# Kernel tuning notes

Measured on AMD Instinct MI355X. Metric: run time of the kernel, lower is better.

Reference implementation:

```python
import jax, jax.numpy as jnp
import numpy as np

B, T, V, E, L, H = 128, 512, 128, 64, 128, 512  # batch, seq, vocab, char_emb, latent, hidden


def setup_inputs() -> dict:
    key = jax.random.key(0)
    ks = jax.random.split(key, 12)
    r = lambda k, shape, s=0.05: jax.random.normal(k, shape, dtype=jnp.float32) * s
    return {
        "char_ids": jax.random.randint(ks[0], (B, T), 0, V),
        "z": jax.random.normal(ks[1], (B, L), dtype=jnp.float32),
        "emb": r(ks[2], (V, E)),
        "cw1": r(ks[3], (L, H)), "cb1": jnp.zeros((H,)), "cg1": jnp.ones((H,)), "cbeta1": jnp.zeros((H,)),
        "cw2": r(ks[4], (H, H)), "cb2": jnp.zeros((H,)), "cg2": jnp.ones((H,)), "cbeta2": jnp.zeros((H,)),
        "wih0": r(ks[5], (4 * H, E + H + 2)), "whh0": r(ks[6], (4 * H, H)),
        "bih0": jnp.zeros((4 * H,)), "bhh0": jnp.zeros((4 * H,)),
        "wih1": r(ks[7], (4 * H, H)), "whh1": r(ks[8], (4 * H, H)),
        "bih1": jnp.zeros((4 * H,)), "bhh1": jnp.zeros((4 * H,)),
        "wo1": r(ks[9], (H, H // 2)), "bo1": jnp.zeros((H // 2,)),
        "wo2": r(ks[10], (H // 2, 2)), "bo2": jnp.zeros((2,)),
        "init_timing": jnp.zeros((2,)),
    }


def _ln(x, g, b, eps=1e-5):
    m = jnp.mean(x, -1, keepdims=True)
    v = jnp.var(x, -1, keepdims=True)
    return (x - m) * jax.lax.rsqrt(v + eps) * g + b


def _lstm_cell(x, h, c, wih, whh, bih, bhh):
    # PyTorch gate order: i, f, g, o
    gates = x @ wih.T + bih + h @ whh.T + bhh
    i, f, g, o = jnp.split(gates, 4, axis=-1)
    c = jax.nn.sigmoid(f) * c + jax.nn.sigmoid(i) * jnp.tanh(g)
    h = jax.nn.sigmoid(o) * jnp.tanh(c)
    return h, c


def reference(char_ids, z, emb, cw1, cb1, cg1, cbeta1, cw2, cb2, cg2, cbeta2,
              wih0, whh0, bih0, bhh0, wih1, whh1, bih1, bhh1,
              wo1, bo1, wo2, bo2, init_timing):
    b = char_ids.shape[0]
    # condition encoder: Linear -> LN -> LeakyReLU(0.2), twice
    cond = jax.nn.leaky_relu(_ln(z @ cw1 + cb1, cg1, cbeta1), 0.2)
    cond = jax.nn.leaky_relu(_ln(cond @ cw2 + cb2, cg2, cbeta2), 0.2)  # (B, H)
    xs = jnp.transpose(emb[char_ids], (1, 0, 2))  # (T, B, E)
    h0 = jnp.zeros((b, H), jnp.float32)
    c0 = jnp.zeros((b, H), jnp.float32)
    h1 = jnp.zeros((b, H), jnp.float32)
    c1 = jnp.zeros((b, H), jnp.float32)
    prev = jnp.broadcast_to(init_timing, (b, 2))

    def step(carry, xt):
        h0, c0, h1, c1, prev = carry
        xin = jnp.concatenate([xt, cond, prev], axis=-1)  # (B, E+H+2)
        h0, c0 = _lstm_cell(xin, h0, c0, wih0, whh0, bih0, bhh0)
        h1, c1 = _lstm_cell(h0, h1, c1, wih1, whh1, bih1, bhh1)
        out = jax.nn.leaky_relu(h1 @ wo1 + bo1, 0.2) @ wo2 + bo2
        out = jax.nn.softplus(out) + 0.005  # (B, 2)
        return (h0, c0, h1, c1, out), out

    _, ys = jax.lax.scan(step, (h0, c0, h1, c1, prev), xs)
    return jnp.transpose(ys, (1, 0, 2))  # (B, T, 2)
```

## Files before the change

### kernel.cpp

```cpp
#include <hip/hip_runtime.h>

#define Bn 128
#define Tn 512
#define Vn 128
#define En 64
#define Ln 128
#define Hn 512
#define G4 2048
#define WGS 256
#define NTHR 512
#define NALL (WGS * NTHR)
#define LSTR 520
#define GRPS 8
#define WPG 32
#define RPG 16

typedef unsigned short u16;
typedef unsigned int u32;
typedef __bf16 bf16x8 __attribute__((ext_vector_type(8)));
typedef float f32x4 __attribute__((ext_vector_type(4)));
typedef u32 u32x4 __attribute__((ext_vector_type(4)));

__device__ inline float bf2f(u16 h) {
    u32 u = ((u32)h) << 16;
    float f;
    __builtin_memcpy(&f, &u, 4);
    return f;
}
__device__ inline u16 f2bf(float f) {
    u32 u;
    __builtin_memcpy(&u, &f, 4);
    u32 r = (u + 0x7fffu + ((u >> 16) & 1u)) >> 16;
    return (u16)r;
}
__device__ inline u32 f2u(float f) { u32 u; __builtin_memcpy(&u, &f, 4); return u; }
__device__ inline float u2f(u32 u) { float f; __builtin_memcpy(&f, &u, 4); return f; }
__device__ inline float sigm(float x) { return 1.f / (1.f + expf(-x)); }
__device__ inline float leaky(float x) { return x > 0.f ? x : 0.2f * x; }
__device__ inline float softplus(float x) {
    return x > 0.f ? x + log1pf(expf(-x)) : log1pf(expf(x));
}

__device__ inline void cload16(const u32* p, u32* w) {
    u32x4 v0, v1, v2, v3;
    asm volatile(
        "global_load_dwordx4 %0, %4, off sc0 sc1\n\t"
        "global_load_dwordx4 %1, %4, off offset:16 sc0 sc1\n\t"
        "global_load_dwordx4 %2, %4, off offset:32 sc0 sc1\n\t"
        "global_load_dwordx4 %3, %4, off offset:48 sc0 sc1\n\t"
        "s_waitcnt vmcnt(0)"
        : "=&v"(v0), "=&v"(v1), "=&v"(v2), "=&v"(v3)
        : "v"(p)
        : "memory");
    *(u32x4*)(w) = v0;
    *(u32x4*)(w + 4) = v1;
    *(u32x4*)(w + 8) = v2;
    *(u32x4*)(w + 12) = v3;
}
__device__ inline u32 cload1(const u32* p) {
    u32 v;
    asm volatile("global_load_dword %0, %1, off sc0 sc1\n\ts_waitcnt vmcnt(0)"
                 : "=v"(v) : "v"(p) : "memory");
    return v;
}
__device__ inline void cwait() { asm volatile("s_waitcnt vmcnt(0)" ::: "memory"); }
__device__ inline void cstore1(u32* p, u32 v) {
    asm volatile("global_store_dword %0, %1, off sc0 sc1" :: "v"(p), "v"(v) : "memory");
}

#define OFF_FLAGS  0x000000
#define OFF_B1SUM  0x002000
#define OFF_WP     0x004000
#define OFF_BIAS0  0x008000
#define OFF_CPAR   0x00A000
#define OFF_H0P    0x010000
#define OFF_H1P    0x050000
#define OFF_PART   0x090000
#define OFF_WO1TH  0x0B0000
#define OFF_WO1TL  0x0F0000
#define OFF_ZF     0x130000
#define OFF_CW1F   0x140000
#define OFF_CW2F   0x180000
#define OFF_CONDF  0x280000
#define OFF_YBUF   0x2C0000
#define OFF_BASE0  0x300000
#define OFF_EMBW   0x400000
#define OFF_W0HI   0x500000
#define OFF_W0LO   0x700000
#define OFF_W1HI   0x900000
#define OFF_W1LO   0xB00000
#define OFF_WI1HI  0xD00000
#define OFF_WI1LO  0xF00000

__device__ inline void gbar_heavy(int* cnt, int* gen) {
    __syncthreads();
    if (threadIdx.x == 0) {
        __threadfence();
        int g = __hip_atomic_load(gen, __ATOMIC_RELAXED, __HIP_MEMORY_SCOPE_AGENT);
        int arrived = __hip_atomic_fetch_add(cnt, 1, __ATOMIC_ACQ_REL, __HIP_MEMORY_SCOPE_AGENT);
        if (arrived == WGS - 1) {
            __hip_atomic_store(cnt, 0, __ATOMIC_RELAXED, __HIP_MEMORY_SCOPE_AGENT);
            __hip_atomic_store(gen, g + 1, __ATOMIC_RELEASE, __HIP_MEMORY_SCOPE_AGENT);
        } else {
            while (__hip_atomic_load(gen, __ATOMIC_ACQUIRE, __HIP_MEMORY_SCOPE_AGENT) == g)
                __builtin_amdgcn_s_sleep(1);
        }
        __threadfence();
    }
    __syncthreads();
}

__device__ inline void poll32(const u32* gf, u32 sq) {
    const int l = threadIdx.x & 31;
    for (;;) {
        u32 v = cload1(gf + l);
        if (__all((int)(v >= sq))) break;
        __builtin_amdgcn_s_sleep(4);
    }
}
__device__ inline void poll16(const u32* gf, u32 sq) {
    const int l = threadIdx.x & 15;
    for (;;) {
        u32 v = cload1(gf + l);
        if (__all((int)(v >= sq))) break;
        __builtin_amdgcn_s_sleep(4);
    }
}

__device__ inline void unpack16(const u32* w, u16* ph, u16* pl) {
    u32 hd[8], ld[8];
#pragma unroll
    for (int i = 0; i < 8; ++i) {
        hd[i] = (w[2 * i] & 0xFFFFu) | (w[2 * i + 1] << 16);
        ld[i] = (w[2 * i] >> 16) | (w[2 * i + 1] & 0xFFFF0000u);
    }
    *(u32x4*)(ph) = *(const u32x4*)(hd);
    *(u32x4*)(ph + 8) = *(const u32x4*)(hd + 4);
    *(u32x4*)(pl) = *(const u32x4*)(ld);
    *(u32x4*)(pl + 8) = *(const u32x4*)(ld + 4);
}

#define MF(a, b, c) __builtin_amdgcn_mfma_f32_16x16x32_bf16(a, b, c, 0, 0, 0)

__device__ inline f32x4 gemm16_3(const u16* __restrict__ Ah, const u16* __restrict__ Al,
                                 const u16* __restrict__ Bhb, const u16* __restrict__ Blb,
                                 int colb, int n, int q) {
    const u16* Bh = Bhb + (size_t)(colb + n) * Hn;
    const u16* Bl = Blb + (size_t)(colb + n) * Hn;
    const int a0 = n * LSTR;
    f32x4 c0 = {0.f, 0.f, 0.f, 0.f}, c1 = c0, c2 = c0;
#pragma unroll 4
    for (int it = 0; it < 16; ++it) {
        const int ko = it * 32 + q * 8;
        bf16x8 bh = *(const bf16x8*)(Bh + ko);
        bf16x8 bl = *(const bf16x8*)(Bl + ko);
        bf16x8 ah = *(const bf16x8*)(Ah + a0 + ko);
        bf16x8 al = *(const bf16x8*)(Al + a0 + ko);
        c0 = MF(ah, bh, c0);
        c1 = MF(al, bh, c1);
        c2 = MF(ah, bl, c2);
    }
    return c0 + c1 + c2;
}

__device__ inline f32x4 gemm16_regB(const u16* __restrict__ Ah, const u16* __restrict__ Al,
                                    const bf16x8* wbh, const bf16x8* wbl, int n, int q) {
    const int a0 = n * LSTR;
    f32x4 c0 = {0.f, 0.f, 0.f, 0.f}, c1 = c0, c2 = c0;
#pragma unroll
    for (int it = 0; it < 16; ++it) {
        const int ko = it * 32 + q * 8;
        bf16x8 ah = *(const bf16x8*)(Ah + a0 + ko);
        bf16x8 al = *(const bf16x8*)(Al + a0 + ko);
        c0 = MF(ah, wbh[it], c0);
        c1 = MF(al, wbh[it], c1);
        c2 = MF(ah, wbl[it], c2);
    }
    return c0 + c1 + c2;
}

__device__ inline f32x4 gemm16_ldsB(const u16* __restrict__ Ah, const u16* __restrict__ Al,
                                    const u16* __restrict__ Bh, const u16* __restrict__ Bl,
                                    int n, int q) {
    const int a0 = n * LSTR;
    f32x4 c0 = {0.f, 0.f, 0.f, 0.f}, c1 = c0, c2 = c0;
#pragma unroll 4
    for (int it = 0; it < 16; ++it) {
        const int ko = it * 32 + q * 8;
        bf16x8 bh = *(const bf16x8*)(Bh + a0 + ko);
        bf16x8 bl = *(const bf16x8*)(Bl + a0 + ko);
        bf16x8 ah = *(const bf16x8*)(Ah + a0 + ko);
        bf16x8 al = *(const bf16x8*)(Al + a0 + ko);
        c0 = MF(ah, bh, c0);
        c1 = MF(al, bh, c1);
        c2 = MF(ah, bl, c2);
    }
    return c0 + c1 + c2;
}

__device__ inline void stage(float* dst, const void* src, int n, int gtid, bool isbf) {
    if (isbf) {
        const u16* s = (const u16*)src;
        for (int e = gtid; e < n; e += NALL) dst[e] = bf2f(s[e]);
    } else {
        const float* s = (const float*)src;
        for (int e = gtid; e < n; e += NALL) dst[e] = s[e];
    }
}
__device__ inline void stage_split(u16* hi, u16* lo, const void* src, int n, int gtid, bool isbf) {
    if (isbf) {
        const u16* s = (const u16*)src;
        for (int e = gtid; e < n; e += NALL) { hi[e] = s[e]; lo[e] = 0; }
    } else {
        const float* s = (const float*)src;
        for (int e = gtid; e < n; e += NALL) {
            float w = s[e];
            u16 h = f2bf(w);
            hi[e] = h;
            lo[e] = f2bf(w - bf2f(h));
        }
    }
}

template <bool ISBF>
__device__ inline float ldw(const void* p, size_t i) {
    if constexpr (ISBF) return bf2f(((const u16*)p)[i]);
    else return ((const float*)p)[i];
}

template <bool ISBF>
__device__ void phase5(const void* wih0, const void* emb, const float* __restrict__ condf,
                       const float* __restrict__ bias0f, float* __restrict__ base0,
                       float* __restrict__ embW, int gtid) {
    const int cc = gtid & 2047;
    const int bb0 = gtid >> 11;
    float b = bias0f[cc];
    float a0 = b, a1 = b, a2 = b, a3 = b;
    const float* c0p = condf + (size_t)bb0 * Hn;
    const float* c1p = condf + (size_t)(bb0 + 32) * Hn;
    const float* c2p = condf + (size_t)(bb0 + 64) * Hn;
    const float* c3p = condf + (size_t)(bb0 + 96) * Hn;
    const size_t wb = (size_t)cc * 578 + 64;
    for (int k = 0; k < Hn; ++k) {
        float w = ldw<ISBF>(wih0, wb + k);
        a0 += c0p[k] * w; a1 += c1p[k] * w; a2 += c2p[k] * w; a3 += c3p[k] * w;
    }
    base0[(size_t)bb0 * G4 + cc] = a0;
    base0[(size_t)(bb0 + 32) * G4 + cc] = a1;
    base0[(size_t)(bb0 + 64) * G4 + cc] = a2;
    base0[(size_t)(bb0 + 96) * G4 + cc] = a3;
    float e0 = 0.f, e1 = 0.f, e2 = 0.f, e3 = 0.f;
    const size_t wb2 = (size_t)cc * 578;
    for (int k = 0; k < En; ++k) {
        float w = ldw<ISBF>(wih0, wb2 + k);
        e0 += ldw<ISBF>(emb, (size_t)bb0 * En + k) * w;
        e1 += ldw<ISBF>(emb, (size_t)(bb0 + 32) * En + k) * w;
        e2 += ldw<ISBF>(emb, (size_t)(bb0 + 64) * En + k) * w;
        e3 += ldw<ISBF>(emb, (size_t)(bb0 + 96) * En + k) * w;
    }
    embW[(size_t)bb0 * G4 + cc] = e0;
    embW[(size_t)(bb0 + 32) * G4 + cc] = e1;
    embW[(size_t)(bb0 + 64) * G4 + cc] = e2;
    embW[(size_t)(bb0 + 96) * G4 + cc] = e3;
}

__device__ inline void ln_leaky_row(const float* __restrict__ x, const float* __restrict__ gamma,
                                    const float* __restrict__ beta, float* __restrict__ out,
                                    float* red) {
    int tid = threadIdx.x;
    float v = x[tid];
    float s = v, s2 = v * v;
    for (int off = 32; off; off >>= 1) {
        s += __shfl_down(s, off);
        s2 += __shfl_down(s2, off);
    }
    int wv = tid >> 6;
    if ((tid & 63) == 0) { red[wv * 2] = s; red[wv * 2 + 1] = s2; }
    __syncthreads();
    if (tid == 0) {
        float ts = 0.f, ts2 = 0.f;
        for (int i = 0; i < 8; ++i) { ts += red[i * 2]; ts2 += red[i * 2 + 1]; }
        float m = ts / 512.f;
        float var = ts2 / 512.f - m * m;
        red[16] = m;
        red[17] = rsqrtf(var + 1e-5f);
    }
    __syncthreads();
    float m = red[16], rs = red[17];
    out[tid] = leaky((v - m) * rs * gamma[tid] + beta[tid]);
    __syncthreads();
}

__global__ void init_flags_kernel(int* flags) { flags[threadIdx.x] = 0; }

__global__ __launch_bounds__(NTHR, 2) void gen_kernel(
    const int* __restrict__ char_ids, const void* z, const void* emb,
    const void* cw1, const void* cb1, const void* cg1, const void* cbeta1,
    const void* cw2, const void* cb2, const void* cg2, const void* cbeta2,
    const void* wih0, const void* whh0, const void* bih0, const void* bhh0,
    const void* wih1, const void* whh1, const void* bih1, const void* bhh1,
    const void* wo1, const void* bo1, const void* wo2, const void* bo2,
    const void* init_t, void* outp, char* __restrict__ ws) {
    __shared__ u16 lh0h[RPG * LSTR];
    __shared__ u16 lh0l[RPG * LSTR];
    __shared__ u16 lh1h[RPG * LSTR];
    __shared__ u16 lh1l[RPG * LSTR];
    __shared__ u16 lwoh[16 * LSTR];
    __shared__ u16 lwol[16 * LSTR];
    __shared__ float smemx[1024];
    __shared__ float pvs[32];
    __shared__ float red[34];

    int* flags = (int*)(ws + OFF_FLAGS);
    float* b1sum = (float*)(ws + OFF_B1SUM);
    float* wpb = (float*)(ws + OFF_WP);
    float* bias0f = (float*)(ws + OFF_BIAS0);
    float* cpar = (float*)(ws + OFF_CPAR);
    u32* h0p = (u32*)(ws + OFF_H0P);
    u32* h1p = (u32*)(ws + OFF_H1P);
    float* partf = (float*)(ws + OFF_PART);
    u16* wo1Th = (u16*)(ws + OFF_WO1TH);
    u16* wo1Tl = (u16*)(ws + OFF_WO1TL);
    float* zf = (float*)(ws + OFF_ZF);
    float* cw1f = (float*)(ws + OFF_CW1F);
    float* cw2f = (float*)(ws + OFF_CW2F);
    float* condf = (float*)(ws + OFF_CONDF);
    float* ybuf = (float*)(ws + OFF_YBUF);
    float* base0 = (float*)(ws + OFF_BASE0);
    float* embW = (float*)(ws + OFF_EMBW);
    u16* W0hi = (u16*)(ws + OFF_W0HI);
    u16* W0lo = (u16*)(ws + OFF_W0LO);
    u16* W1hi = (u16*)(ws + OFF_W1HI);
    u16* W1lo = (u16*)(ws + OFF_W1LO);
    u16* Wi1hi = (u16*)(ws + OFF_WI1HI);
    u16* Wi1lo = (u16*)(ws + OFF_WI1LO);
    float* wo1f = base0;

    const bool isbf = (((const u32*)cg1)[0] == 0x3F803F80u);

    const int g = blockIdx.x;
    const int tid = threadIdx.x;
    const int wv = tid >> 6;
    const int grp = g >> 5;
    const int ut = g & 31;
    const int mat = wv >> 2;
    const int gw = wv & 3;
    const int R0g = grp * RPG;
    const int colb = gw * 512 + ut * 16;
    const int lane = tid & 63;
    const int n = lane & 15;
    const int q = lane >> 4;
    const int gtid = g * NTHR + tid;
    const f32x4 Z4 = {0.f, 0.f, 0.f, 0.f};

    u32* gf = (u32*)flags + grp * 64;
    u32* gf2 = (u32*)flags + grp * 64 + 32;
    u32* gfl = gf + ut;
    int* hcnt = flags + 512;
    int* hgen = flags + 528;
    float* part = partf + grp * 1024;

    stage_split(W0hi, W0lo, whh0, G4 * Hn, gtid, isbf);
    stage_split(W1hi, W1lo, whh1, G4 * Hn, gtid, isbf);
    stage_split(Wi1hi, Wi1lo, wih1, G4 * Hn, gtid, isbf);
    stage(zf, z, Bn * Ln, gtid, isbf);
    stage(cw1f, cw1, Ln * Hn, gtid, isbf);
    stage(cw2f, cw2, Hn * Hn, gtid, isbf);
    stage(cpar + 0, cg1, 512, gtid, isbf);
    stage(cpar + 512, cbeta1, 512, gtid, isbf);
    stage(cpar + 1024, cg2, 512, gtid, isbf);
    stage(cpar + 1536, cbeta2, 512, gtid, isbf);
    stage(cpar + 2048, bo1, 256, gtid, isbf);
    stage(cpar + 2304, bo2, 2, gtid, isbf);
    stage(cpar + 2560, cb2, 512, gtid, isbf);
    stage(cpar + 3072, cb1, 512, gtid, isbf);
    stage(cpar + 3584, wo2, 256 * 2, gtid, isbf);
    stage(wo1f, wo1, Hn * 256, gtid, isbf);
    if (gtid < Bn * Hn) { cstore1(h0p + gtid, 0); cstore1(h1p + gtid, 0); }
    if (isbf) {
        if (gtid < G4) b1sum[gtid] = bf2f(((const u16*)bih1)[gtid]) + bf2f(((const u16*)bhh1)[gtid]);
        if (gtid < G4) bias0f[gtid] = bf2f(((const u16*)bih0)[gtid]) + bf2f(((const u16*)bhh0)[gtid]);
        if (gtid < 4096) {
            size_t ix = (size_t)(gtid >> 1) * 578 + 576 + (gtid & 1);
            wpb[gtid] = bf2f(((const u16*)wih0)[ix]);
        }
    } else {
        if (gtid < G4) b1sum[gtid] = ((const float*)bih1)[gtid] + ((const float*)bhh1)[gtid];
        if (gtid < G4) bias0f[gtid] = ((const float*)bih0)[gtid] + ((const float*)bhh0)[gtid];
        if (gtid < 4096) {
            size_t ix = (size_t)(gtid >> 1) * 578 + 576 + (gtid & 1);
            wpb[gtid] = ((const float*)wih0)[ix];
        }
    }
    gbar_heavy(hcnt, hgen);
    if (gtid < Bn * Hn) {
        int bb = gtid >> 9, nn = gtid & 511;
        float a = cpar[3072 + nn];
        const float* zr = zf + bb * Ln;
        for (int k = 0; k < Ln; ++k) a += zr[k] * cw1f[k * Hn + nn];
        ybuf[gtid] = a;
    }
    for (int e = gtid; e < 256 * Hn; e += NALL) {
        int nn = e >> 9, kk = e & 511;
        float w = wo1f[kk * 256 + nn];
        u16 hv = f2bf(w);
        wo1Th[e] = hv;
        wo1Tl[e] = f2bf(w - bf2f(hv));
    }
    gbar_heavy(hcnt, hgen);
    if (g < Bn) ln_leaky_row(ybuf + g * Hn, cpar + 0, cpar + 512, condf + g * Hn, red);
    gbar_heavy(hcnt, hgen);
    if (g < Bn) {
        float a = cpar[2560 + tid];
        const float* crow = condf + g * Hn;
        for (int k = 0; k < Hn; ++k) a += crow[k] * cw2f[k * Hn + tid];
        ybuf[g * Hn + tid] = a;
    }
    gbar_heavy(hcnt, hgen);
    if (g < Bn) ln_leaky_row(ybuf + g * Hn, cpar + 1024, cpar + 1536, condf + g * Hn, red);
    gbar_heavy(hcnt, hgen);
    if (gtid < Bn * Hn) {
        if (isbf) phase5<true>(wih0, emb, condf, bias0f, base0, embW, gtid);
        else phase5<false>(wih0, emb, condf, bias0f, base0, embW, gtid);
    }
    gbar_heavy(hcnt, hgen);

    bf16x8 wbh[16], wbl[16];
    {
        const u16* Bh = (mat == 0 ? W0hi : W1hi) + (size_t)(colb + n) * Hn;
        const u16* Bl = (mat == 0 ? W0lo : W1lo) + (size_t)(colb + n) * Hn;
#pragma unroll
        for (int it = 0; it < 16; ++it) {
            wbh[it] = *(const bf16x8*)(Bh + it * 32 + q * 8);
            wbl[it] = *(const bf16x8*)(Bl + it * 32 + q * 8);
        }
    }
    const bool headwg = (ut < 16);
    if (headwg) {
        for (int e = tid; e < 16 * Hn; e += NTHR) {
            int col = e >> 9, k = e & 511;
            lwoh[col * LSTR + k] = wo1Th[(size_t)(ut * 16 + col) * Hn + k];
            lwol[col * LSTR + k] = wo1Tl[(size_t)(ut * 16 + col) * Hn + k];
        }
    }

    float c0 = 0.f, c1 = 0.f;
    const int lr = tid >> 4;
    const int un = tid & 15;
    const int bb = R0g + lr;
    const int uu = ut * 16 + un;
    const float* bo1f = cpar + 2048;
    const float* bo2f = cpar + 2304;
    const float* wo2f = cpar + 3584;
    const int srow = tid >> 5;
    const int blk = tid & 31;
    const int kub = blk * 16;
    f32x4 acc1c = Z4;

    for (int e = tid; e < RPG * LSTR; e += NTHR) {
        lh0h[e] = 0; lh0l[e] = 0; lh1h[e] = 0; lh1l[e] = 0;
    }
    if (tid < 32) pvs[tid] = isbf ? bf2f(((const u16*)init_t)[tid & 1])
                                  : ((const float*)init_t)[tid & 1];

    for (int t = 0; t < Tn; ++t) {
        if (t >= 1) {
            if (wv == 0) poll32(gf, 2 * (u32)t);
            __syncthreads();
            if (blk != ut) {
                u32 w[16];
                cload16(h1p + (size_t)(R0g + srow) * Hn + kub, w);
                unpack16(w, lh1h + srow * LSTR + kub, lh1l + srow * LSTR + kub);
            }
        }
        __syncthreads();
        if (headwg && wv == 0 && t >= 1) {
            f32x4 ha = gemm16_ldsB(lh1h, lh1l, lwoh, lwol, n, q);
            float p[4][2];
#pragma unroll
            for (int r = 0; r < 4; ++r) {
                float hv = leaky(ha[r] + bo1f[ut * 16 + n]);
                p[r][0] = hv * wo2f[(ut * 16 + n) * 2];
                p[r][1] = hv * wo2f[(ut * 16 + n) * 2 + 1];
            }
#pragma unroll
            for (int r = 0; r < 4; ++r)
#pragma unroll
                for (int j = 0; j < 2; ++j) {
                    float s = p[r][j];
                    s += __shfl_xor(s, 1, 16);
                    s += __shfl_xor(s, 2, 16);
                    s += __shfl_xor(s, 4, 16);
                    s += __shfl_xor(s, 8, 16);
                    p[r][j] = s;
                }
            if (n == 0) {
#pragma unroll
                for (int r = 0; r < 4; ++r)
#pragma unroll
                    for (int j = 0; j < 2; ++j) {
                        int row = q * 4 + r;
                        cstore1((u32*)(part + (row * 2 + j) * 16 + ut), f2u(p[r][j]));
                    }
            }
            cwait();
            if (tid == 0) cstore1(gf2 + ut, (u32)t);
        }
        if (mat == 0) {
            f32x4 a = gemm16_regB(lh0h, lh0l, wbh, wbl, n, q);
#pragma unroll
            for (int r = 0; r < 4; ++r)
                smemx[gw * 256 + (q * 4 + r) * 16 + n] = a[r];
        } else {
            acc1c = gemm16_regB(lh1h, lh1l, wbh, wbl, n, q);
        }
        if (t >= 1) {
            if (wv == 0) {
                poll16(gf2, (u32)t);
                if (tid < 32) {
                    int row = tid >> 1, j = tid & 1;
                    u32 hw[16];
                    cload16((const u32*)(part + (row * 2 + j) * 16), hw);
                    float s = bo2f[j];
#pragma unroll
                    for (int i = 0; i < 16; ++i) s += u2f(hw[i]);
                    float y = softplus(s) + 0.005f;
                    pvs[row * 2 + j] = y;
                    if (ut == 0) {
                        size_t oi = ((size_t)(R0g + row) * Tn + (t - 1)) * 2 + j;
                        if (isbf) ((u16*)outp)[oi] = f2bf(y);
                        else ((float*)outp)[oi] = y;
                    }
                }
            }
        }
        __syncthreads();
        if (tid < 256) {
            int id = char_ids[bb * Tn + t];
            float pv0 = pvs[lr * 2], pv1 = pvs[lr * 2 + 1];
            float gv[4];
#pragma unroll
            for (int gi = 0; gi < 4; ++gi) {
                int cc = gi * 512 + uu;
                gv[gi] = smemx[gi * 256 + lr * 16 + un] + base0[(size_t)bb * G4 + cc] +
                         embW[(size_t)id * G4 + cc] + pv0 * wpb[2 * cc] + pv1 * wpb[2 * cc + 1];
            }
            float ig = sigm(gv[0]), fg = sigm(gv[1]), gg = tanhf(gv[2]), og = sigm(gv[3]);
            c0 = fg * c0 + ig * gg;
            float h = og * tanhf(c0);
            u16 hv = f2bf(h);
            u16 lv = f2bf(h - bf2f(hv));
            lh0h[lr * LSTR + uu] = hv;
            lh0l[lr * LSTR + uu] = lv;
            cstore1(h0p + (size_t)bb * Hn + uu, (u32)hv | ((u32)lv << 16));
        }
        cwait();
        __syncthreads();
        if (tid == 0) cstore1(gfl, 2 * (u32)t + 1);

        if (wv == 0) poll32(gf, 2 * (u32)t + 1);
        __syncthreads();
        if (blk != ut) {
            u32 w[16];
            cload16(h0p + (size_t)(R0g + srow) * Hn + kub, w);
            unpack16(w, lh0h + srow * LSTR + kub, lh0l + srow * LSTR + kub);
        }
        __syncthreads();
        if (mat == 1) {
            f32x4 a = gemm16_3(lh0h, lh0l, Wi1hi, Wi1lo, colb, n, q);
            acc1c = acc1c + a;
#pragma unroll
            for (int r = 0; r < 4; ++r)
                smemx[gw * 256 + (q * 4 + r) * 16 + n] = acc1c[r];
        }
        __syncthreads();
        if (tid < 256) {
            float gv[4];
#pragma unroll
            for (int gi = 0; gi < 4; ++gi) {
                int cc = gi * 512 + uu;
                gv[gi] = smemx[gi * 256 + lr * 16 + un] + b1sum[cc];
            }
            float ig = sigm(gv[0]), fg = sigm(gv[1]), gg = tanhf(gv[2]), og = sigm(gv[3]);
            c1 = fg * c1 + ig * gg;
            float h = og * tanhf(c1);
            u16 hv = f2bf(h);
            u16 lv = f2bf(h - bf2f(hv));
            lh1h[lr * LSTR + uu] = hv;
            lh1l[lr * LSTR + uu] = lv;
            cstore1(h1p + (size_t)bb * Hn + uu, (u32)hv | ((u32)lv << 16));
        }
        cwait();
        __syncthreads();
        if (tid == 0) cstore1(gfl, 2 * (u32)t + 2);
    }

    if (wv == 0) poll32(gf, 2 * (u32)Tn);
    __syncthreads();
    if (blk != ut) {
        u32 w[16];
        cload16(h1p + (size_t)(R0g + srow) * Hn + kub, w);
        unpack16(w, lh1h + srow * LSTR + kub, lh1l + srow * LSTR + kub);
    }
    __syncthreads();
    if (headwg && wv == 0) {
        f32x4 ha = gemm16_ldsB(lh1h, lh1l, lwoh, lwol, n, q);
        float p[4][2];
#pragma unroll
        for (int r = 0; r < 4; ++r) {
            float hv = leaky(ha[r] + bo1f[ut * 16 + n]);
            p[r][0] = hv * wo2f[(ut * 16 + n) * 2];
            p[r][1] = hv * wo2f[(ut * 16 + n) * 2 + 1];
        }
#pragma unroll
        for (int r = 0; r < 4; ++r)
#pragma unroll
            for (int j = 0; j < 2; ++j) {
                float s = p[r][j];
                s += __shfl_xor(s, 1, 16);
                s += __shfl_xor(s, 2, 16);
                s += __shfl_xor(s, 4, 16);
                s += __shfl_xor(s, 8, 16);
                p[r][j] = s;
            }
        if (n == 0) {
#pragma unroll
            for (int r = 0; r < 4; ++r)
#pragma unroll
                for (int j = 0; j < 2; ++j) {
                    int row = q * 4 + r;
                    cstore1((u32*)(part + (row * 2 + j) * 16 + ut), f2u(p[r][j]));
                }
        }
        cwait();
        if (tid == 0) cstore1(gf2 + ut, (u32)Tn);
    }
    if (ut == 0 && wv == 0) {
        poll16(gf2, (u32)Tn);
        if (tid < 32) {
            int row = tid >> 1, j = tid & 1;
            u32 hw[16];
            cload16((const u32*)(part + (row * 2 + j) * 16), hw);
            float s = bo2f[j];
#pragma unroll
            for (int i = 0; i < 16; ++i) s += u2f(hw[i]);
            float y = softplus(s) + 0.005f;
            size_t oi = ((size_t)(R0g + row) * Tn + (Tn - 1)) * 2 + j;
            if (isbf) ((u16*)outp)[oi] = f2bf(y);
            else ((float*)outp)[oi] = y;
        }
    }
}

extern "C" void kernel_launch(void* const* d_in, const int* in_sizes, int n_in,
                              void* d_out, int out_size, void* d_ws, size_t ws_size,
                              hipStream_t stream) {
    (void)in_sizes; (void)n_in; (void)out_size; (void)ws_size;
    init_flags_kernel<<<1, 1024, 0, stream>>>((int*)d_ws);
    gen_kernel<<<WGS, NTHR, 0, stream>>>(
        (const int*)d_in[0], d_in[1], d_in[2], d_in[3], d_in[4], d_in[5], d_in[6], d_in[7],
        d_in[8], d_in[9], d_in[10], d_in[11], d_in[12], d_in[13], d_in[14], d_in[15], d_in[16],
        d_in[17], d_in[18], d_in[19], d_in[20], d_in[21], d_in[22], d_in[23],
        d_out, (char*)d_ws);
}
```

Baseline: 8.805 ms.

## Specialize bf16 path: keep all weights in registers, drop lo-weight MFMAs, remap groups

When inputs are bf16, the weight lo halves are zero, so the MFMA against the weight lo part is skipped. The freed register slot now holds Wi1 (for layer-1 waves) or the wo1 head weights, instead of streaming Wi1 from global memory and wo1 from LDS each step. It also remaps workgroups so the 8 row groups are interleaved across block indices, and moves the output-head reduction from wave 0 to wave 4 to balance work. The fp32 path keeps the old three-MFMA scheme.

Result: slower. 10.19 ms (+15.7%).

```diff
diff --git a/kernel.cpp b/kernel.cpp
--- a/kernel.cpp
+++ b/kernel.cpp
@@ -163,8 +163,8 @@
     return c0 + c1 + c2;
 }
 
-__device__ inline f32x4 gemm16_regB(const u16* __restrict__ Ah, const u16* __restrict__ Al,
-                                    const bf16x8* wbh, const bf16x8* wbl, int n, int q) {
+__device__ inline f32x4 gemm16_regB3(const u16* __restrict__ Ah, const u16* __restrict__ Al,
+                                     const bf16x8* wa, const bf16x8* wb, int n, int q) {
     const int a0 = n * LSTR;
     f32x4 c0 = {0.f, 0.f, 0.f, 0.f}, c1 = c0, c2 = c0;
 #pragma unroll
@@ -172,16 +172,31 @@
         const int ko = it * 32 + q * 8;
         bf16x8 ah = *(const bf16x8*)(Ah + a0 + ko);
         bf16x8 al = *(const bf16x8*)(Al + a0 + ko);
-        c0 = MF(ah, wbh[it], c0);
-        c1 = MF(al, wbh[it], c1);
-        c2 = MF(ah, wbl[it], c2);
+        c0 = MF(ah, wa[it], c0);
+        c1 = MF(al, wa[it], c1);
+        c2 = MF(ah, wb[it], c2);
     }
     return c0 + c1 + c2;
 }
 
-__device__ inline f32x4 gemm16_ldsB(const u16* __restrict__ Ah, const u16* __restrict__ Al,
-                                    const u16* __restrict__ Bh, const u16* __restrict__ Bl,
-                                    int n, int q) {
+__device__ inline f32x4 gemm16_regB2(const u16* __restrict__ Ah, const u16* __restrict__ Al,
+                                     const bf16x8* wb, int n, int q) {
+    const int a0 = n * LSTR;
+    f32x4 c0 = {0.f, 0.f, 0.f, 0.f}, c1 = c0;
+#pragma unroll
+    for (int it = 0; it < 16; ++it) {
+        const int ko = it * 32 + q * 8;
+        bf16x8 ah = *(const bf16x8*)(Ah + a0 + ko);
+        bf16x8 al = *(const bf16x8*)(Al + a0 + ko);
+        c0 = MF(ah, wb[it], c0);
+        c1 = MF(al, wb[it], c1);
+    }
+    return c0 + c1;
+}
+
+__device__ inline f32x4 gemm16_ldsB3(const u16* __restrict__ Ah, const u16* __restrict__ Al,
+                                     const u16* __restrict__ Bh, const u16* __restrict__ Bl,
+                                     int n, int q) {
     const int a0 = n * LSTR;
     f32x4 c0 = {0.f, 0.f, 0.f, 0.f}, c1 = c0, c2 = c0;
 #pragma unroll 4
@@ -341,8 +356,8 @@
     const int g = blockIdx.x;
     const int tid = threadIdx.x;
     const int wv = tid >> 6;
-    const int grp = g >> 5;
-    const int ut = g & 31;
+    const int grp = g & 7;
+    const int ut = g >> 3;
     const int mat = wv >> 2;
     const int gw = wv & 3;
     const int R0g = grp * RPG;
@@ -425,18 +440,25 @@
     }
     gbar_heavy(hcnt, hgen);
 
-    bf16x8 wbh[16], wbl[16];
+    const bool headwg = (ut < 16);
+    bf16x8 wA[16], wB[16];
     {
-        const u16* Bh = (mat == 0 ? W0hi : W1hi) + (size_t)(colb + n) * Hn;
-        const u16* Bl = (mat == 0 ? W0lo : W1lo) + (size_t)(colb + n) * Hn;
+        const u16* BhA = (mat == 0 ? W0hi : W1hi) + (size_t)(colb + n) * Hn;
+        const u16* BhB;
+        if (isbf) {
+            if (mat == 1) BhB = Wi1hi + (size_t)(colb + n) * Hn;
+            else if (headwg && wv == 0) BhB = wo1Th + (size_t)(ut * 16 + n) * Hn;
+            else BhB = BhA;
+        } else {
+            BhB = (mat == 0 ? W0lo : W1lo) + (size_t)(colb + n) * Hn;
+        }
 #pragma unroll
         for (int it = 0; it < 16; ++it) {
-            wbh[it] = *(const bf16x8*)(Bh + it * 32 + q * 8);
-            wbl[it] = *(const bf16x8*)(Bl + it * 32 + q * 8);
-        }
-    }
-    const bool headwg = (ut < 16);
-    if (headwg) {
+            wA[it] = *(const bf16x8*)(BhA + it * 32 + q * 8);
+            wB[it] = *(const bf16x8*)(BhB + it * 32 + q * 8);
+        }
+    }
+    if (!isbf && headwg) {
         for (int e = tid; e < 16 * Hn; e += NTHR) {
             int col = e >> 9, k = e & 511;
             lwoh[col * LSTR + k] = wo1Th[(size_t)(ut * 16 + col) * Hn + k];
@@ -475,7 +497,8 @@
         }
         __syncthreads();
         if (headwg && wv == 0 && t >= 1) {
-            f32x4 ha = gemm16_ldsB(lh1h, lh1l, lwoh, lwol, n, q);
+            f32x4 ha = isbf ? gemm16_regB2(lh1h, lh1l, wB, n, q)
+                            : gemm16_ldsB3(lh1h, lh1l, lwoh, lwol, n, q);
             float p[4][2];
 #pragma unroll
             for (int r = 0; r < 4; ++r) {
@@ -507,30 +530,31 @@
             if (tid == 0) cstore1(gf2 + ut, (u32)t);
         }
         if (mat == 0) {
-            f32x4 a = gemm16_regB(lh0h, lh0l, wbh, wbl, n, q);
+            f32x4 a = isbf ? gemm16_regB2(lh0h, lh0l, wA, n, q)
+                           : gemm16_regB3(lh0h, lh0l, wA, wB, n, q);
 #pragma unroll
             for (int r = 0; r < 4; ++r)
                 smemx[gw * 256 + (q * 4 + r) * 16 + n] = a[r];
         } else {
-            acc1c = gemm16_regB(lh1h, lh1l, wbh, wbl, n, q);
-        }
-        if (t >= 1) {
-            if (wv == 0) {
-                poll16(gf2, (u32)t);
-                if (tid < 32) {
-                    int row = tid >> 1, j = tid & 1;
-                    u32 hw[16];
-                    cload16((const u32*)(part + (row * 2 + j) * 16), hw);
-                    float s = bo2f[j];
-#pragma unroll
-                    for (int i = 0; i < 16; ++i) s += u2f(hw[i]);
-                    float y = softplus(s) + 0.005f;
-                    pvs[row * 2 + j] = y;
-                    if (ut == 0) {
-                        size_t oi = ((size_t)(R0g + row) * Tn + (t - 1)) * 2 + j;
-                        if (isbf) ((u16*)outp)[oi] = f2bf(y);
-                        else ((float*)outp)[oi] = y;
-                    }
+            acc1c = isbf ? gemm16_regB2(lh1h, lh1l, wA, n, q)
+                         : gemm16_regB3(lh1h, lh1l, wA, wB, n, q);
+        }
+        if (t >= 1 && wv == 4) {
+            poll16(gf2, (u32)t);
+            if (tid < 288) {
+                int l = tid - 256;
+                int row = l >> 1, j = l & 1;
+                u32 hw[16];
+                cload16((const u32*)(part + (row * 2 + j) * 16), hw);
+                float s = bo2f[j];
+#pragma unroll
+                for (int i = 0; i < 16; ++i) s += u2f(hw[i]);
+                float y = softplus(s) + 0.005f;
+                pvs[row * 2 + j] = y;
+                if (ut == 0) {
+                    size_t oi = ((size_t)(R0g + row) * Tn + (t - 1)) * 2 + j;
+                    if (isbf) ((u16*)outp)[oi] = f2bf(y);
+                    else ((float*)outp)[oi] = y;
                 }
             }
         }
@@ -567,7 +591,8 @@
         }
         __syncthreads();
         if (mat == 1) {
-            f32x4 a = gemm16_3(lh0h, lh0l, Wi1hi, Wi1lo, colb, n, q);
+            f32x4 a = isbf ? gemm16_regB2(lh0h, lh0l, wB, n, q)
+                           : gemm16_3(lh0h, lh0l, Wi1hi, Wi1lo, colb, n, q);
             acc1c = acc1c + a;
 #pragma unroll
             for (int r = 0; r < 4; ++r)
@@ -604,7 +629,8 @@
     }
     __syncthreads();
     if (headwg && wv == 0) {
-        f32x4 ha = gemm16_ldsB(lh1h, lh1l, lwoh, lwol, n, q);
+        f32x4 ha = isbf ? gemm16_regB2(lh1h, lh1l, wB, n, q)
+                        : gemm16_ldsB3(lh1h, lh1l, lwoh, lwol, n, q);
         float p[4][2];
 #pragma unroll
         for (int r = 0; r < 4; ++r) {
```
